# Kernel optimization log

Hardware: AMD Instinct MI355X
Metric: run time of the kernel (lower is better)

## Reference

```python
import jax, jax.numpy as jnp
import numpy as np

N0, IN, H = 262144, 128, 32
N1, N2 = 131072, 65536
E0, E1 = 2097152, 1048576
EPS = 1e-12


def _sage_conv(x_src, x_tgt, src, tgt, n_tgt, wl, bl, wr):
    # mean-aggregate neighbor features: scatter-add then divide by counts
    msg = x_src[src]                                        # [E, F] gather
    agg = jax.ops.segment_sum(msg, tgt, num_segments=n_tgt) # [n_tgt, F]
    cnt = jax.ops.segment_sum(jnp.ones((src.shape[0],), x_src.dtype), tgt,
                              num_segments=n_tgt)
    mean = agg / jnp.maximum(cnt, 1.0)[:, None]
    out = mean @ wl.T + bl + x_tgt @ wr.T                   # lin_l(agg) + lin_r(root)
    # normalize=True -> L2 normalize rows
    norm = jnp.maximum(jnp.linalg.norm(out, axis=-1, keepdims=True), EPS)
    return out / norm


def setup_inputs() -> dict:
    key = jax.random.key(0)
    ks = jax.random.split(key, 10)
    s = 1.0 / np.sqrt(IN)
    sh = 1.0 / np.sqrt(H)
    return {
        "x": jax.random.normal(ks[0], (N0, IN), jnp.float32),
        "src0": jax.random.randint(ks[1], (E0,), 0, N0),
        "tgt0": jax.random.randint(ks[2], (E0,), 0, N1),
        "src1": jax.random.randint(ks[3], (E1,), 0, N1),
        "tgt1": jax.random.randint(ks[4], (E1,), 0, N2),
        "wl0": jax.random.normal(ks[5], (H, IN), jnp.float32) * s,
        "bl0": jnp.zeros((H,), jnp.float32),
        "wr0": jax.random.normal(ks[6], (H, IN), jnp.float32) * s,
        "wl1": jax.random.normal(ks[7], (H, H), jnp.float32) * sh,
        "bl1": jnp.zeros((H,), jnp.float32),
        "wr1": jax.random.normal(ks[8], (H, H), jnp.float32) * sh,
        "n1": N1,
        "n2": N2,
    }


def reference(x, src0, tgt0, src1, tgt1, wl0, bl0, wr0, wl1, bl1, wr1, n1, n2):
    # layer 0: bipartite (x[:N0] sources -> first n1 nodes are targets)
    h = _sage_conv(x, x[:n1], src0, tgt0, n1, wl0, bl0, wr0)
    h = jax.nn.relu(h)
    # layer 1 (last layer: no relu)
    out = _sage_conv(h, h[:n2], src1, tgt1, n2, wl1, bl1, wr1)
    return out
```

## Files before the change

### kernel.cpp

```cpp
#include <hip/hip_runtime.h>

#define N0c 262144
#define INc 128
#define Hc  32
#define N1c 131072
#define N2c 65536
#define E0c 2097152
#define E1c 1048576
#define CAPc 4608

__device__ __forceinline__ void fma4(float4& a, float s, const float4 w) {
    a.x = fmaf(s, w.x, a.x);
    a.y = fmaf(s, w.y, a.y);
    a.z = fmaf(s, w.z, a.z);
    a.w = fmaf(s, w.w, a.w);
}

__global__ __launch_bounds__(256) void lin0_one_kernel(
    const float* __restrict__ x, const float* __restrict__ w,
    float* __restrict__ out)
{
    __shared__ float xs[128 * 32];
    __shared__ float ws[32 * 32];
    const int t = threadIdx.x;
    const int rowBase = blockIdx.x * 128;
    const int cg = t & 7;
    const int rg = t >> 3;

    float4* xs4w = (float4*)xs;
    const float4* xs4 = (const float4*)xs;
    const float4* ws4 = (const float4*)ws;

    float4 acc[4];
#pragma unroll
    for (int i = 0; i < 4; ++i) acc[i] = make_float4(0.f, 0.f, 0.f, 0.f);

    for (int kc = 0; kc < 4; ++kc) {
        if (kc) __syncthreads();
#pragma unroll
        for (int i = 0; i < 4; ++i) {
            int idx = t + 256 * i;
            int row = idx >> 3, kq = idx & 7;
            float4 v = ((const float4*)x)[(rowBase + row) * 32 + kc * 8 + kq];
            xs4w[row * 8 + ((kq + (row >> 2)) & 7)] = v;
        }
#pragma unroll
        for (int i = 0; i < 4; ++i) {
            int idx = t + 256 * i;
            int kk = idx & 31, j = idx >> 5;
            int dst = kk * 32 + 4 * (((j >> 2) + kk) & 7) + (j & 3);
            ws[dst] = w[j * 128 + kc * 32 + kk];
        }
        __syncthreads();

#pragma unroll
        for (int kq = 0; kq < 8; ++kq) {
            float4 xv[4];
#pragma unroll
            for (int i = 0; i < 4; ++i)
                xv[i] = xs4[(4 * rg + i) * 8 + ((kq + rg) & 7)];
            const int kb = 4 * kq;
            float4 w0 = ws4[(kb + 0) * 8 + ((cg + kb + 0) & 7)];
            float4 w1 = ws4[(kb + 1) * 8 + ((cg + kb + 1) & 7)];
            float4 w2 = ws4[(kb + 2) * 8 + ((cg + kb + 2) & 7)];
            float4 w3 = ws4[(kb + 3) * 8 + ((cg + kb + 3) & 7)];
#pragma unroll
            for (int i = 0; i < 4; ++i) {
                fma4(acc[i], xv[i].x, w0);
                fma4(acc[i], xv[i].y, w1);
                fma4(acc[i], xv[i].z, w2);
                fma4(acc[i], xv[i].w, w3);
            }
        }
    }

#pragma unroll
    for (int i = 0; i < 4; ++i) {
        int r = rowBase + 4 * rg + i;
        ((float4*)out)[r * 8 + cg] = acc[i];
    }
}

__global__ __launch_bounds__(128) void lin1_kernel(
    const float* __restrict__ h, const float* __restrict__ wl,
    const float* __restrict__ wr, float* __restrict__ y, float* __restrict__ z)
{
    __shared__ float xs[64 * 32];
    __shared__ float wls[32 * 32];
    __shared__ float wrs[32 * 32];
    const int t = threadIdx.x;
    const long rowBase = (long)blockIdx.x * 64;
    const bool doZ = rowBase < N2c;

#pragma unroll
    for (int i = 0; i < 8; ++i) {
        int idx = t + 128 * i;
        int j = idx >> 5, k = idx & 31;
        int dst = k * 32 + 4 * (((j >> 2) + k) & 7) + (j & 3);
        wls[dst] = wl[idx];
        if (doZ) wrs[dst] = wr[idx];
    }
#pragma unroll
    for (int i = 0; i < 4; ++i) {
        int idx = t + 128 * i;
        int row = idx >> 3, k4 = idx & 7;
        float4 v = ((const float4*)h)[rowBase * 8 + idx];
        ((float4*)xs)[row * 8 + ((k4 + (row >> 2)) & 7)] = v;
    }
    __syncthreads();

    const int cg = t & 7;
    const int rg = t >> 3;
    const float4* xs4  = (const float4*)xs;
    const float4* wls4 = (const float4*)wls;
    const float4* wrs4 = (const float4*)wrs;

    float4 accY[4], accZ[4];
#pragma unroll
    for (int i = 0; i < 4; ++i) {
        accY[i] = make_float4(0.f, 0.f, 0.f, 0.f);
        accZ[i] = make_float4(0.f, 0.f, 0.f, 0.f);
    }

#pragma unroll
    for (int k4 = 0; k4 < 8; ++k4) {
        float4 xv[4];
#pragma unroll
        for (int i = 0; i < 4; ++i)
            xv[i] = xs4[(4 * rg + i) * 8 + ((k4 + rg) & 7)];
        const int kb = 4 * k4;
        float4 w0 = wls4[(kb + 0) * 8 + ((cg + kb + 0) & 7)];
        float4 w1 = wls4[(kb + 1) * 8 + ((cg + kb + 1) & 7)];
        float4 w2 = wls4[(kb + 2) * 8 + ((cg + kb + 2) & 7)];
        float4 w3 = wls4[(kb + 3) * 8 + ((cg + kb + 3) & 7)];
#pragma unroll
        for (int i = 0; i < 4; ++i) {
            fma4(accY[i], xv[i].x, w0);
            fma4(accY[i], xv[i].y, w1);
            fma4(accY[i], xv[i].z, w2);
            fma4(accY[i], xv[i].w, w3);
        }
        if (doZ) {
            float4 u0 = wrs4[(kb + 0) * 8 + ((cg + kb + 0) & 7)];
            float4 u1 = wrs4[(kb + 1) * 8 + ((cg + kb + 1) & 7)];
            float4 u2 = wrs4[(kb + 2) * 8 + ((cg + kb + 2) & 7)];
            float4 u3 = wrs4[(kb + 3) * 8 + ((cg + kb + 3) & 7)];
#pragma unroll
            for (int i = 0; i < 4; ++i) {
                fma4(accZ[i], xv[i].x, u0);
                fma4(accZ[i], xv[i].y, u1);
                fma4(accZ[i], xv[i].z, u2);
                fma4(accZ[i], xv[i].w, u3);
            }
        }
    }
#pragma unroll
    for (int i = 0; i < 4; ++i) {
        long r = rowBase + 4 * rg + i;
        ((float4*)y)[r * 8 + cg] = accY[i];
        if (doZ) ((float4*)z)[r * 8 + cg] = accZ[i];
    }
}

__global__ __launch_bounds__(512) void part_kernel(
    const int* __restrict__ src0, const int* __restrict__ tgt0,
    const int* __restrict__ src1, const int* __restrict__ tgt1,
    int* __restrict__ pairs0, int* __restrict__ pairs1,
    int* __restrict__ bcur0, int* __restrict__ bcur1)
{
    __shared__ int hist[512];
    __shared__ int bb[512];
    const int t = threadIdx.x;
    const int* src; const int* tgt; int* pairs; int* bcur; int base4;
    if (blockIdx.x < E0c / 8192) {
        src = src0; tgt = tgt0; pairs = pairs0; bcur = bcur0;
        base4 = blockIdx.x * 2048;
    } else {
        src = src1; tgt = tgt1; pairs = pairs1; bcur = bcur1;
        base4 = (blockIdx.x - E0c / 8192) * 2048;
    }

    hist[t] = 0;
    __syncthreads();
    int4 tv[4];
#pragma unroll
    for (int i = 0; i < 4; ++i) {
        tv[i] = ((const int4*)tgt)[base4 + i * 512 + t];
        atomicAdd(&hist[tv[i].x >> 8], 1);
        atomicAdd(&hist[tv[i].y >> 8], 1);
        atomicAdd(&hist[tv[i].z >> 8], 1);
        atomicAdd(&hist[tv[i].w >> 8], 1);
    }
    __syncthreads();
    bb[t] = hist[t] ? atomicAdd(&bcur[t], hist[t]) : 0;
    __syncthreads();
    hist[t] = 0;
    __syncthreads();
#pragma unroll
    for (int i = 0; i < 4; ++i) {
        int4 sv = ((const int4*)src)[base4 + i * 512 + t];
        int b, r, slot;
        b = tv[i].x >> 8; r = atomicAdd(&hist[b], 1); slot = bb[b] + r;
        if (slot < CAPc) pairs[b * CAPc + slot] = (sv.x << 8) | (tv[i].x & 255);
        b = tv[i].y >> 8; r = atomicAdd(&hist[b], 1); slot = bb[b] + r;
        if (slot < CAPc) pairs[b * CAPc + slot] = (sv.y << 8) | (tv[i].y & 255);
        b = tv[i].z >> 8; r = atomicAdd(&hist[b], 1); slot = bb[b] + r;
        if (slot < CAPc) pairs[b * CAPc + slot] = (sv.z << 8) | (tv[i].z & 255);
        b = tv[i].w >> 8; r = atomicAdd(&hist[b], 1); slot = bb[b] + r;
        if (slot < CAPc) pairs[b * CAPc + slot] = (sv.w << 8) | (tv[i].w & 255);
    }
}

__global__ __launch_bounds__(512) void sortb_kernel(
    const int* __restrict__ pairs, const int* __restrict__ bcur,
    int* __restrict__ cnt, int* __restrict__ cur, int* __restrict__ eidx)
{
    __shared__ int cl[256];
    __shared__ int offs[256];
    const int b = blockIdx.x;
    const int t = threadIdx.x;
    const int tlo = b << 8;
    const int beg = b * CAPc;
    int n = bcur[b]; if (n > CAPc) n = CAPc;
    const int end = beg + n;

    if (t < 256) cl[t] = 0;
    __syncthreads();
    for (int e = beg + t; e < end; e += 512)
        atomicAdd(&cl[pairs[e] & 255], 1);
    __syncthreads();
    int local = 0;
    if (t < 256) { local = cl[t]; offs[t] = local; }
    __syncthreads();
    int v = local;
#pragma unroll
    for (int off = 1; off < 256; off <<= 1) {
        int u = (t < 256 && t >= off) ? offs[t - off] : 0;
        __syncthreads();
        if (t < 256) { v += u; offs[t] = v; }
        __syncthreads();
    }
    if (t < 256) {
        int ex = v - local;
        cnt[tlo + t] = local;
        cur[tlo + t] = beg + ex;
        offs[t] = beg + ex;
        cl[t] = 0;
    }
    __syncthreads();
    for (int e = beg + t; e < end; e += 512) {
        int p = pairs[e];
        int li = p & 255;
        int r = atomicAdd(&cl[li], 1);
        eidx[offs[li] + r] = p >> 8;
    }
}

__global__ __launch_bounds__(256) void gather_agg_kernel(
    const float* __restrict__ yv, const int* __restrict__ eidx,
    const int* __restrict__ cnt, const int* __restrict__ cur,
    const float* z, const float* __restrict__ b,
    float* out, int n, int doRelu)
{
    int t = blockIdx.x * 256 + threadIdx.x;
    int row = t >> 3, part = t & 7;
    if (row >= n) return;
    int c = cnt[row];
    int beg = cur[row];
    int end = beg + c;
    const float4* y4 = (const float4*)yv;
    float4 acc = make_float4(0.f, 0.f, 0.f, 0.f);
    int e = beg;
    for (; e + 3 < end; e += 4) {
        int s0 = eidx[e], s1 = eidx[e + 1], s2 = eidx[e + 2], s3 = eidx[e + 3];
        float4 v0 = y4[(long)s0 * 8 + part];
        float4 v1 = y4[(long)s1 * 8 + part];
        float4 v2 = y4[(long)s2 * 8 + part];
        float4 v3 = y4[(long)s3 * 8 + part];
        acc.x += (v0.x + v1.x) + (v2.x + v3.x);
        acc.y += (v0.y + v1.y) + (v2.y + v3.y);
        acc.z += (v0.z + v1.z) + (v2.z + v3.z);
        acc.w += (v0.w + v1.w) + (v2.w + v3.w);
    }
    for (; e < end; ++e) {
        int s0 = eidx[e];
        float4 v0 = y4[(long)s0 * 8 + part];
        acc.x += v0.x; acc.y += v0.y; acc.z += v0.z; acc.w += v0.w;
    }
    float inv = 1.f / fmaxf((float)c, 1.f);
    float4 bb = ((const float4*)b)[part];
    float4 zz = ((const float4*)z)[(long)row * 8 + part];
    float4 v;
    v.x = fmaf(acc.x, inv, bb.x) + zz.x;
    v.y = fmaf(acc.y, inv, bb.y) + zz.y;
    v.z = fmaf(acc.z, inv, bb.z) + zz.z;
    v.w = fmaf(acc.w, inv, bb.w) + zz.w;
    float ss = v.x * v.x + v.y * v.y + v.z * v.z + v.w * v.w;
    ss += __shfl_xor(ss, 1);
    ss += __shfl_xor(ss, 2);
    ss += __shfl_xor(ss, 4);
    float q = 1.f / fmaxf(sqrtf(ss), 1e-12f);
    v.x *= q; v.y *= q; v.z *= q; v.w *= q;
    if (doRelu) {
        v.x = fmaxf(v.x, 0.f); v.y = fmaxf(v.y, 0.f);
        v.z = fmaxf(v.z, 0.f); v.w = fmaxf(v.w, 0.f);
    }
    ((float4*)out)[(long)row * 8 + part] = v;
}

extern "C" void kernel_launch(void* const* d_in, const int* in_sizes, int n_in,
                              void* d_out, int out_size, void* d_ws, size_t ws_size,
                              hipStream_t stream) {
    const float* x   = (const float*)d_in[0];
    const int* src0  = (const int*)d_in[1];
    const int* tgt0  = (const int*)d_in[2];
    const int* src1  = (const int*)d_in[3];
    const int* tgt1  = (const int*)d_in[4];
    const float* wl0 = (const float*)d_in[5];
    const float* bl0 = (const float*)d_in[6];
    const float* wr0 = (const float*)d_in[7];
    const float* wl1 = (const float*)d_in[8];
    const float* bl1 = (const float*)d_in[9];
    const float* wr1 = (const float*)d_in[10];

    char* W = (char*)d_ws;
    float* y0    = (float*)(W + 0);
    float* y1    = (float*)(W + 0);
    float* z1    = (float*)(W + 16777216);
    float* z0    = (float*)(W + 33554432);
    float* h     = (float*)(W + 33554432);
    int*   pairs0= (int*)  (W + 50331648);
    int*   pairs1= (int*)  (W + 59768832);
    int*   eidx0 = (int*)  (W + 64487424);
    int*   eidx1 = (int*)  (W + 50331648);
    int*   cnt0  = (int*)  (W + 73924608);
    int*   cur0  = (int*)  (W + 74448896);
    int*   cnt1  = (int*)  (W + 74973184);
    int*   cur1  = (int*)  (W + 75235328);
    int*   bcur0 = (int*)  (W + 75497472);
    int*   bcur1 = (int*)  (W + 75499520);

    hipMemsetAsync(bcur0, 0, 3072, stream);
    lin0_one_kernel<<<N0c / 128, 256, 0, stream>>>(x, wl0, y0);
    lin0_one_kernel<<<N1c / 128, 256, 0, stream>>>(x, wr0, z0);

    part_kernel<<<E0c / 8192 + E1c / 8192, 512, 0, stream>>>(
        src0, tgt0, src1, tgt1, pairs0, pairs1, bcur0, bcur1);

    sortb_kernel<<<N1c / 256, 512, 0, stream>>>(pairs0, bcur0, cnt0, cur0, eidx0);
    gather_agg_kernel<<<(N1c * 8) / 256, 256, 0, stream>>>(
        y0, eidx0, cnt0, cur0, z0, bl0, h, N1c, 1);

    sortb_kernel<<<N2c / 256, 512, 0, stream>>>(pairs1, bcur1, cnt1, cur1, eidx1);
    lin1_kernel<<<N1c / 64, 128, 0, stream>>>(h, wl1, wr1, y1, z1);
    gather_agg_kernel<<<(N2c * 8) / 256, 256, 0, stream>>>(
        y1, eidx1, cnt1, cur1, z1, bl1, (float*)d_out, N2c, 0);
}
```

Baseline: 408.5 us.

## Merge lin0 and sortb launches, deepen gather unroll with dual accumulators

The two layer-0 linear launches become one grid that picks weights and output by block index. The two bucket-sort launches are merged the same way, which needs eidx1 moved to a non-overlapping workspace region. The gather-aggregate loop is unrolled to 8 loads with two accumulators, and the root and bias loads are hoisted ahead of the loop so more memory requests are in flight. The aim is to cut launch gaps and tail underuse and to hide gather latency, at the cost of a larger workspace and more registers.

```diff
diff --git a/kernel.cpp b/kernel.cpp
--- a/kernel.cpp
+++ b/kernel.cpp
@@ -16,14 +16,23 @@
     a.w = fmaf(s, w.w, a.w);
 }
 
-__global__ __launch_bounds__(256) void lin0_one_kernel(
-    const float* __restrict__ x, const float* __restrict__ w,
-    float* __restrict__ out)
+__device__ __forceinline__ void add4(float4& a, const float4 v) {
+    a.x += v.x; a.y += v.y; a.z += v.z; a.w += v.w;
+}
+
+__global__ __launch_bounds__(256) void lin0_both_kernel(
+    const float* __restrict__ x, const float* __restrict__ wl,
+    const float* __restrict__ wr, float* __restrict__ y, float* __restrict__ z)
 {
     __shared__ float xs[128 * 32];
     __shared__ float ws[32 * 32];
     const int t = threadIdx.x;
-    const int rowBase = blockIdx.x * 128;
+    const float* w; float* out; int rowBase;
+    if (blockIdx.x < N0c / 128) {
+        w = wl; out = y; rowBase = blockIdx.x * 128;
+    } else {
+        w = wr; out = z; rowBase = (blockIdx.x - N0c / 128) * 128;
+    }
     const int cg = t & 7;
     const int rg = t >> 3;
 
@@ -212,13 +221,22 @@
 }
 
 __global__ __launch_bounds__(512) void sortb_kernel(
-    const int* __restrict__ pairs, const int* __restrict__ bcur,
-    int* __restrict__ cnt, int* __restrict__ cur, int* __restrict__ eidx)
+    const int* __restrict__ pairs0, const int* __restrict__ bcur0,
+    int* __restrict__ cnt0, int* __restrict__ cur0, int* __restrict__ eidx0,
+    const int* __restrict__ pairs1, const int* __restrict__ bcur1,
+    int* __restrict__ cnt1, int* __restrict__ cur1, int* __restrict__ eidx1)
 {
     __shared__ int cl[256];
     __shared__ int offs[256];
-    const int b = blockIdx.x;
     const int t = threadIdx.x;
+    const int* pairs; const int* bcur; int* cnt; int* cur; int* eidx; int b;
+    if (blockIdx.x < N1c / 256) {
+        b = blockIdx.x;
+        pairs = pairs0; bcur = bcur0; cnt = cnt0; cur = cur0; eidx = eidx0;
+    } else {
+        b = blockIdx.x - N1c / 256;
+        pairs = pairs1; bcur = bcur1; cnt = cnt1; cur = cur1; eidx = eidx1;
+    }
     const int tlo = b << 8;
     const int beg = b * CAPc;
     int n = bcur[b]; if (n > CAPc) n = CAPc;
@@ -268,33 +286,43 @@
     int c = cnt[row];
     int beg = cur[row];
     int end = beg + c;
+    float4 zz = ((const float4*)z)[(long)row * 8 + part];
+    float4 bb = ((const float4*)b)[part];
     const float4* y4 = (const float4*)yv;
-    float4 acc = make_float4(0.f, 0.f, 0.f, 0.f);
+    float4 accA = make_float4(0.f, 0.f, 0.f, 0.f);
+    float4 accB = make_float4(0.f, 0.f, 0.f, 0.f);
     int e = beg;
-    for (; e + 3 < end; e += 4) {
-        int s0 = eidx[e], s1 = eidx[e + 1], s2 = eidx[e + 2], s3 = eidx[e + 3];
+    for (; e + 7 < end; e += 8) {
+        int s0 = eidx[e],     s1 = eidx[e + 1], s2 = eidx[e + 2], s3 = eidx[e + 3];
+        int s4 = eidx[e + 4], s5 = eidx[e + 5], s6 = eidx[e + 6], s7 = eidx[e + 7];
         float4 v0 = y4[(long)s0 * 8 + part];
         float4 v1 = y4[(long)s1 * 8 + part];
         float4 v2 = y4[(long)s2 * 8 + part];
         float4 v3 = y4[(long)s3 * 8 + part];
-        acc.x += (v0.x + v1.x) + (v2.x + v3.x);
-        acc.y += (v0.y + v1.y) + (v2.y + v3.y);
-        acc.z += (v0.z + v1.z) + (v2.z + v3.z);
-        acc.w += (v0.w + v1.w) + (v2.w + v3.w);
-    }
-    for (; e < end; ++e) {
-        int s0 = eidx[e];
+        float4 v4 = y4[(long)s4 * 8 + part];
+        float4 v5 = y4[(long)s5 * 8 + part];
+        float4 v6 = y4[(long)s6 * 8 + part];
+        float4 v7 = y4[(long)s7 * 8 + part];
+        add4(accA, v0); add4(accB, v1); add4(accA, v2); add4(accB, v3);
+        add4(accA, v4); add4(accB, v5); add4(accA, v6); add4(accB, v7);
+    }
+    for (; e + 1 < end; e += 2) {
+        int s0 = eidx[e], s1 = eidx[e + 1];
         float4 v0 = y4[(long)s0 * 8 + part];
-        acc.x += v0.x; acc.y += v0.y; acc.z += v0.z; acc.w += v0.w;
-    }
+        float4 v1 = y4[(long)s1 * 8 + part];
+        add4(accA, v0); add4(accB, v1);
+    }
+    if (e < end) {
+        float4 v0 = y4[(long)eidx[e] * 8 + part];
+        add4(accA, v0);
+    }
+    add4(accA, accB);
     float inv = 1.f / fmaxf((float)c, 1.f);
-    float4 bb = ((const float4*)b)[part];
-    float4 zz = ((const float4*)z)[(long)row * 8 + part];
     float4 v;
-    v.x = fmaf(acc.x, inv, bb.x) + zz.x;
-    v.y = fmaf(acc.y, inv, bb.y) + zz.y;
-    v.z = fmaf(acc.z, inv, bb.z) + zz.z;
-    v.w = fmaf(acc.w, inv, bb.w) + zz.w;
+    v.x = fmaf(accA.x, inv, bb.x) + zz.x;
+    v.y = fmaf(accA.y, inv, bb.y) + zz.y;
+    v.z = fmaf(accA.z, inv, bb.z) + zz.z;
+    v.w = fmaf(accA.w, inv, bb.w) + zz.w;
     float ss = v.x * v.x + v.y * v.y + v.z * v.z + v.w * v.w;
     ss += __shfl_xor(ss, 1);
     ss += __shfl_xor(ss, 2);
@@ -332,26 +360,28 @@
     int*   pairs0= (int*)  (W + 50331648);
     int*   pairs1= (int*)  (W + 59768832);
     int*   eidx0 = (int*)  (W + 64487424);
-    int*   eidx1 = (int*)  (W + 50331648);
-    int*   cnt0  = (int*)  (W + 73924608);
-    int*   cur0  = (int*)  (W + 74448896);
-    int*   cnt1  = (int*)  (W + 74973184);
-    int*   cur1  = (int*)  (W + 75235328);
-    int*   bcur0 = (int*)  (W + 75497472);
-    int*   bcur1 = (int*)  (W + 75499520);
+    int*   eidx1 = (int*)  (W + 73924608);
+    int*   cnt0  = (int*)  (W + 78643200);
+    int*   cur0  = (int*)  (W + 79167488);
+    int*   cnt1  = (int*)  (W + 79691776);
+    int*   cur1  = (int*)  (W + 79953920);
+    int*   bcur0 = (int*)  (W + 80216064);
+    int*   bcur1 = (int*)  (W + 80218112);
 
     hipMemsetAsync(bcur0, 0, 3072, stream);
-    lin0_one_kernel<<<N0c / 128, 256, 0, stream>>>(x, wl0, y0);
-    lin0_one_kernel<<<N1c / 128, 256, 0, stream>>>(x, wr0, z0);
+    lin0_both_kernel<<<N0c / 128 + N1c / 128, 256, 0, stream>>>(
+        x, wl0, wr0, y0, z0);
 
     part_kernel<<<E0c / 8192 + E1c / 8192, 512, 0, stream>>>(
         src0, tgt0, src1, tgt1, pairs0, pairs1, bcur0, bcur1);
 
-    sortb_kernel<<<N1c / 256, 512, 0, stream>>>(pairs0, bcur0, cnt0, cur0, eidx0);
+    sortb_kernel<<<N1c / 256 + N2c / 256, 512, 0, stream>>>(
+        pairs0, bcur0, cnt0, cur0, eidx0,
+        pairs1, bcur1, cnt1, cur1, eidx1);
+
     gather_agg_kernel<<<(N1c * 8) / 256, 256, 0, stream>>>(
         y0, eidx0, cnt0, cur0, z0, bl0, h, N1c, 1);
 
-    sortb_kernel<<<N2c / 256, 512, 0, stream>>>(pairs1, bcur1, cnt1, cur1, eidx1);
     lin1_kernel<<<N1c / 64, 128, 0, stream>>>(h, wl1, wr1, y1, z1);
     gather_agg_kernel<<<(N2c * 8) / 256, 256, 0, stream>>>(
         y1, eidx1, cnt1, cur1, z1, bl1, (float*)d_out, N2c, 0);
```

New measurement: 393.4 us. 1.04x faster.
